# Optimization experiments

Measured on AMD Instinct MI355X. Metric: run time of the kernel, lower is better.

## Reference

```python
import jax, jax.numpy as jnp
import numpy as np

C, PH, PW, H, W = 10, 7, 7, 34, 34
STRIDE = 8.0
S = 4  # sample_per_part


def setup_inputs() -> dict:
    key = jax.random.key(0)
    k1, k2, k3, k4, k5 = jax.random.split(key, 5)
    N = 30000
    ft = jax.random.normal(k1, (1, C * PH * PW, H, W), dtype=jnp.float32)
    x1 = jax.random.uniform(k2, (N,), dtype=jnp.float32) * 200.0
    y1 = jax.random.uniform(k3, (N,), dtype=jnp.float32) * 200.0
    bw = jax.random.uniform(k4, (N,), dtype=jnp.float32) * 70.0 + 2.0
    bh = jax.random.uniform(k5, (N,), dtype=jnp.float32) * 70.0 + 2.0
    rois = jnp.stack([jnp.zeros((N,), jnp.float32), x1, y1, x1 + bw, y1 + bh], axis=1)
    return {"ft_add_left_right": ft, "rois": rois}


def reference(ft_add_left_right, rois):
    ft = ft_add_left_right[0].reshape(C, PH, PW, H, W)
    roi_start_w = rois[:, 1] / STRIDE
    roi_start_h = rois[:, 2] / STRIDE
    roi_end_w = rois[:, 3] / STRIDE
    roi_end_h = rois[:, 4] / STRIDE
    # torch.threshold(x, 0.1, 0.1): x if x > 0.1 else 0.1
    roi_height = jnp.where(roi_end_h - roi_start_h > 0.1, roi_end_h - roi_start_h, 0.1)
    roi_width = jnp.where(roi_end_w - roi_start_w > 0.1, roi_end_w - roi_start_w, 0.1)
    bin_size_h = roi_height / PH
    bin_size_w = roi_width / PW
    sub_h = bin_size_h / S
    sub_w = bin_size_w / S

    gh, gw = jnp.meshgrid(jnp.arange(PH), jnp.arange(PW), indexing='ij')
    phs = gh.reshape(-1, 1)  # [49,1]
    pws = gw.reshape(-1, 1)  # [49,1]
    hstart = jnp.floor(roi_start_h + phs * bin_size_h)  # [49,N]
    wstart = jnp.floor(roi_start_w + pws * bin_size_w)  # [49,N]

    N = rois.shape[0]
    sum_ = jnp.zeros((C, PH * PW, N), jnp.float32)
    count = jnp.zeros((PH * PW, N), jnp.float32)

    for ih in range(S):
        for iw in range(S):
            w = wstart + (iw + 0.5) * sub_w  # [49,N]
            h = hstart + (ih + 0.5) * sub_h
            keep = (w > -1) & (w < W) & (h > -1) & (h < H)
            x1 = jnp.floor(w).astype(jnp.int32)
            x2 = jnp.ceil(w).astype(jnp.int32)
            y1 = jnp.floor(h).astype(jnp.int32)
            y2 = jnp.ceil(h).astype(jnp.int32)
            x1v = (x1 >= 0) & (x1 < W)
            x2v = (x2 >= 0) & (x2 < W)
            y1v = (y1 >= 0) & (y1 < H)
            y2v = (y2 >= 0) & (y2 < H)
            x1 = jnp.clip(x1, 0, W - 1)
            x2 = jnp.clip(x2, 0, W - 1)
            y1 = jnp.clip(y1, 0, H - 1)
            y2 = jnp.clip(y2, 0, H - 1)
            dist_x = w - x1
            dist_y = h - y1
            # gathers: result [C,49,N]
            v11 = ft[:, phs, pws, y1, x1]
            v12 = ft[:, phs, pws, y2, x1]
            v21 = ft[:, phs, pws, y1, x2]
            v22 = ft[:, phs, pws, y2, x2]
            # faithful to source: ALL four masks zero value11 only (source bug)
            bad11 = (~x1v & y1v) | (~x1v & y2v) | (~x2v & y1v) | (~x2v & y2v)
            v11 = jnp.where(bad11, 0.0, v11)
            value = ((1 - dist_x) * (1 - dist_y) * v11
                     + (1 - dist_x) * dist_y * v12
                     + dist_x * (1 - dist_y) * v21
                     + dist_x * dist_y * v22)
            sum_ = sum_ + jnp.where(keep, value, 0.0)
            count = count + keep.astype(jnp.float32)

    out = jnp.where(count > 0, sum_ / jnp.maximum(count, 1.0), sum_)
    return jnp.transpose(out, (2, 0, 1))  # [N, C, 49]
```

## Files before the change

### kernel.cpp

```cpp
#include <hip/hip_runtime.h>


#define NC 10
#define NBIN 49
#define FH 34
#define FW 34
#define PLANE (FH * FW)
#define CSTRIDE 16
#define RPB 16
#define TSTRIDE 491

__global__ __launch_bounds__(256) void prep_kernel(
    const float* __restrict__ ft, float* __restrict__ ftT)
{
    const int p = blockIdx.x * 256 + threadIdx.x;
    if (p >= NBIN * PLANE) return;
    float v[NC];
#pragma unroll
    for (int c = 0; c < NC; ++c) v[c] = ft[c * (NBIN * PLANE) + p];
    float4* d = reinterpret_cast<float4*>(ftT + (size_t)p * CSTRIDE);
    d[0] = make_float4(v[0], v[1], v[2], v[3]);
    d[1] = make_float4(v[4], v[5], v[6], v[7]);
    d[2] = make_float4(v[8], v[9], 0.f, 0.f);
}

__global__ __launch_bounds__(256) void main_kernel(
    const float* __restrict__ rois, const float* __restrict__ ftT,
    const float* __restrict__ ft, float* __restrict__ out, int N, int use_t)
{
    __shared__ float tile[RPB][TSTRIDE];

    const int r = threadIdx.x & (RPB - 1);
    const int s = threadIdx.x >> 4;
    const int n = blockIdx.x * RPB + r;
    const bool valid = (n < N);

    float rsw = 0.f, rsh = 0.f, rew = 0.f, reh = 0.f;
    if (valid) {
        rsw = rois[n * 5 + 1] * 0.125f;
        rsh = rois[n * 5 + 2] * 0.125f;
        rew = rois[n * 5 + 3] * 0.125f;
        reh = rois[n * 5 + 4] * 0.125f;
    }
    float rheight = __fsub_rn(reh, rsh);
    if (!(rheight > 0.1f)) rheight = 0.1f;
    float rwidth = __fsub_rn(rew, rsw);
    if (!(rwidth > 0.1f)) rwidth = 0.1f;
    const float bsh   = __fdiv_rn(rheight, 7.0f);
    const float bsw   = __fdiv_rn(rwidth, 7.0f);
    const float sub_h = __fdiv_rn(bsh, 4.0f);
    const float sub_w = __fdiv_rn(bsw, 4.0f);

#pragma unroll
    for (int j = 0; j < 4; ++j) {
        const int bin = j * 16 + s;
        if (valid && bin < NBIN) {
            const int ph = bin / 7;
            const int pw = bin - ph * 7;
            const float hstart = floorf(__fadd_rn(rsh, __fmul_rn((float)ph, bsh)));
            const float wstart = floorf(__fadd_rn(rsw, __fmul_rn((float)pw, bsw)));

            float AY[3] = {0.f, 0.f, 0.f}, BY[3] = {0.f, 0.f, 0.f};
            float cntY = 0.f;
            int Y0 = 0;
#pragma unroll
            for (int ih = 0; ih < 4; ++ih) {
                const float h = __fadd_rn(hstart, __fmul_rn((float)ih + 0.5f, sub_h));
                const bool hok = (h > -1.0f) && (h < (float)FH);
                const int y1 = (int)floorf(h);
                const int y2 = (int)ceilf(h);
                const bool y1v = (y1 >= 0) && (y1 < FH);
                const bool y2v = (y2 >= 0) && (y2 < FH);
                const int y1c = min(max(y1, 0), FH - 1);
                const int y2c = min(max(y2, 0), FH - 1);
                const float dy = __fsub_rn(h, (float)y1c);
                if (ih == 0) Y0 = y1c;
                const int i1 = y1c - Y0, i2 = y2c - Y0;
                const float t1 = hok ? (1.0f - dy) : 0.0f;
                const float t2 = hok ? dy : 0.0f;
                const float tb = (hok && (y1v || y2v)) ? (1.0f - dy) : 0.0f;
                cntY += hok ? 1.0f : 0.0f;
#pragma unroll
                for (int p = 0; p < 3; ++p) {
                    AY[p] += (i1 == p) ? t1 : 0.0f;
                    AY[p] += (i2 == p) ? t2 : 0.0f;
                    BY[p] += (i1 == p) ? tb : 0.0f;
                }
            }

            float AX[3] = {0.f, 0.f, 0.f}, BX[3] = {0.f, 0.f, 0.f};
            float cntX = 0.f;
            int X0 = 0;
#pragma unroll
            for (int iw = 0; iw < 4; ++iw) {
                const float w = __fadd_rn(wstart, __fmul_rn((float)iw + 0.5f, sub_w));
                const bool wok = (w > -1.0f) && (w < (float)FW);
                const int x1 = (int)floorf(w);
                const int x2 = (int)ceilf(w);
                const bool x1v = (x1 >= 0) && (x1 < FW);
                const bool x2v = (x2 >= 0) && (x2 < FW);
                const int x1c = min(max(x1, 0), FW - 1);
                const int x2c = min(max(x2, 0), FW - 1);
                const float dx = __fsub_rn(w, (float)x1c);
                if (iw == 0) X0 = x1c;
                const int i1 = x1c - X0, i2 = x2c - X0;
                const float t1 = wok ? (1.0f - dx) : 0.0f;
                const float t2 = wok ? dx : 0.0f;
                const float tb = (wok && ((!x1v) || (!x2v))) ? (1.0f - dx) : 0.0f;
                cntX += wok ? 1.0f : 0.0f;
#pragma unroll
                for (int q = 0; q < 3; ++q) {
                    AX[q] += (i1 == q) ? t1 : 0.0f;
                    AX[q] += (i2 == q) ? t2 : 0.0f;
                    BX[q] += (i1 == q) ? tb : 0.0f;
                }
            }

            float sum[NC];
#pragma unroll
            for (int c = 0; c < NC; ++c) sum[c] = 0.f;

            const int binbase = bin * PLANE;
#pragma unroll
            for (int p = 0; p < 3; ++p) {
                const int py = min(Y0 + p, FH - 1);
#pragma unroll
                for (int q = 0; q < 3; ++q) {
                    const int px = min(X0 + q, FW - 1);
                    const float wgt = AY[p] * AX[q] - BY[p] * BX[q];
                    if (wgt != 0.0f) {
                        if (use_t) {
                            const float* pix = ftT + (size_t)(binbase + py * FW + px) * CSTRIDE;
                            const float4 a  = *(const float4*)pix;
                            const float4 b  = *(const float4*)(pix + 4);
                            const float2 c2 = *(const float2*)(pix + 8);
                            sum[0] += wgt * a.x;  sum[1] += wgt * a.y;
                            sum[2] += wgt * a.z;  sum[3] += wgt * a.w;
                            sum[4] += wgt * b.x;  sum[5] += wgt * b.y;
                            sum[6] += wgt * b.z;  sum[7] += wgt * b.w;
                            sum[8] += wgt * c2.x; sum[9] += wgt * c2.y;
                        } else {
                            const int off = binbase + py * FW + px;
#pragma unroll
                            for (int c = 0; c < NC; ++c)
                                sum[c] += wgt * ft[c * (NBIN * PLANE) + off];
                        }
                    }
                }
            }

            const float cnt = cntY * cntX;
            const float inv = (cnt > 0.0f) ? __fdiv_rn(1.0f, cnt) : 1.0f;
            float* tp = &tile[r][0];
#pragma unroll
            for (int c = 0; c < NC; ++c) tp[c * NBIN + bin] = sum[c] * inv;
        }
    }

    __syncthreads();

    const int n0 = blockIdx.x * RPB;
    for (int i = threadIdx.x; i < RPB * (NC * NBIN); i += 256) {
        const int row = i / (NC * NBIN);
        const int col = i - row * (NC * NBIN);
        const int n2 = n0 + row;
        if (n2 < N) out[(size_t)n2 * (NC * NBIN) + col] = tile[row][col];
    }
}

extern "C" void kernel_launch(void* const* d_in, const int* in_sizes, int n_in,
                              void* d_out, int out_size, void* d_ws, size_t ws_size,
                              hipStream_t stream) {
    const float* ft   = (const float*)d_in[0];
    const float* rois = (const float*)d_in[1];
    float* out        = (float*)d_out;
    const int N = in_sizes[1] / 5;

    const size_t need = (size_t)NBIN * PLANE * CSTRIDE * sizeof(float);
    const int use_t = (ws_size >= need) ? 1 : 0;
    float* ftT = (float*)d_ws;

    if (use_t) {
        const int npix = NBIN * PLANE;
        prep_kernel<<<(npix + 255) / 256, 256, 0, stream>>>(ft, ftT);
    }
    main_kernel<<<(N + RPB - 1) / RPB, 256, 0, stream>>>(rois, ftT, ft, out, N, use_t);
}
```

Measured before the change: 129.0 us.

## Share per-row/column interpolation weights via LDS and issue branchless gathers

```diff
diff --git a/kernel.cpp b/kernel.cpp
--- a/kernel.cpp
+++ b/kernel.cpp
@@ -9,6 +9,7 @@
 #define CSTRIDE 16
 #define RPB 16
 #define TSTRIDE 491
+#define NSIDE 14
 
 __global__ __launch_bounds__(256) void prep_kernel(
     const float* __restrict__ ft, float* __restrict__ ftT)
@@ -28,6 +29,7 @@
     const float* __restrict__ rois, const float* __restrict__ ftT,
     const float* __restrict__ ft, float* __restrict__ out, int N, int use_t)
 {
+    __shared__ float sides[NSIDE][RPB][8];
     __shared__ float tile[RPB][TSTRIDE];
 
     const int r = threadIdx.x & (RPB - 1);
@@ -51,101 +53,116 @@
     const float sub_h = __fdiv_rn(bsh, 4.0f);
     const float sub_w = __fdiv_rn(bsw, 4.0f);
 
+    if (s < NSIDE) {
+        const bool isY = (s < 7);
+        const int  k   = isY ? s : s - 7;
+        const float st = isY ? rsh : rsw;
+        const float bs = isY ? bsh : bsw;
+        const float sb = isY ? sub_h : sub_w;
+        const float start = floorf(__fadd_rn(st, __fmul_rn((float)k, bs)));
+
+        float A[3] = {0.f, 0.f, 0.f}, B[3] = {0.f, 0.f, 0.f};
+        float cnt = 0.f;
+        int P0 = 0;
+#pragma unroll
+        for (int i = 0; i < 4; ++i) {
+            const float h = __fadd_rn(start, __fmul_rn((float)i + 0.5f, sb));
+            const bool ok = (h > -1.0f) && (h < 34.0f);
+            const int p1 = (int)floorf(h);
+            const int p2 = (int)ceilf(h);
+            const bool v1 = (p1 >= 0) && (p1 < 34);
+            const bool v2 = (p2 >= 0) && (p2 < 34);
+            const int p1c = min(max(p1, 0), 33);
+            const int p2c = min(max(p2, 0), 33);
+            const float d = __fsub_rn(h, (float)p1c);
+            if (i == 0) P0 = p1c;
+            const int i1 = p1c - P0, i2 = p2c - P0;
+            const float t1 = ok ? (1.0f - d) : 0.0f;
+            const float t2 = ok ? d : 0.0f;
+            const bool bsel = isY ? (v1 || v2) : ((!v1) || (!v2));
+            const float tb = (ok && bsel) ? (1.0f - d) : 0.0f;
+            cnt += ok ? 1.0f : 0.0f;
+#pragma unroll
+            for (int p = 0; p < 3; ++p) {
+                A[p] += (i1 == p) ? t1 : 0.0f;
+                A[p] += (i2 == p) ? t2 : 0.0f;
+                B[p] += (i1 == p) ? tb : 0.0f;
+            }
+        }
+        float* sp = &sides[s][r][0];
+        sp[0] = A[0]; sp[1] = A[1]; sp[2] = A[2];
+        sp[3] = B[0]; sp[4] = B[1]; sp[5] = B[2];
+        sp[6] = cnt;  sp[7] = (float)P0;
+    }
+    __syncthreads();
+
 #pragma unroll
     for (int j = 0; j < 4; ++j) {
-        const int bin = j * 16 + s;
+        const int bin = j * RPB + s;
         if (valid && bin < NBIN) {
             const int ph = bin / 7;
             const int pw = bin - ph * 7;
-            const float hstart = floorf(__fadd_rn(rsh, __fmul_rn((float)ph, bsh)));
-            const float wstart = floorf(__fadd_rn(rsw, __fmul_rn((float)pw, bsw)));
-
-            float AY[3] = {0.f, 0.f, 0.f}, BY[3] = {0.f, 0.f, 0.f};
-            float cntY = 0.f;
-            int Y0 = 0;
-#pragma unroll
-            for (int ih = 0; ih < 4; ++ih) {
-                const float h = __fadd_rn(hstart, __fmul_rn((float)ih + 0.5f, sub_h));
-                const bool hok = (h > -1.0f) && (h < (float)FH);
-                const int y1 = (int)floorf(h);
-                const int y2 = (int)ceilf(h);
-                const bool y1v = (y1 >= 0) && (y1 < FH);
-                const bool y2v = (y2 >= 0) && (y2 < FH);
-                const int y1c = min(max(y1, 0), FH - 1);
-                const int y2c = min(max(y2, 0), FH - 1);
-                const float dy = __fsub_rn(h, (float)y1c);
-                if (ih == 0) Y0 = y1c;
-                const int i1 = y1c - Y0, i2 = y2c - Y0;
-                const float t1 = hok ? (1.0f - dy) : 0.0f;
-                const float t2 = hok ? dy : 0.0f;
-                const float tb = (hok && (y1v || y2v)) ? (1.0f - dy) : 0.0f;
-                cntY += hok ? 1.0f : 0.0f;
-#pragma unroll
-                for (int p = 0; p < 3; ++p) {
-                    AY[p] += (i1 == p) ? t1 : 0.0f;
-                    AY[p] += (i2 == p) ? t2 : 0.0f;
-                    BY[p] += (i1 == p) ? tb : 0.0f;
+
+            const float4 ya = *(const float4*)&sides[ph][r][0];
+            const float4 yb = *(const float4*)&sides[ph][r][4];
+            const float4 xa = *(const float4*)&sides[7 + pw][r][0];
+            const float4 xb = *(const float4*)&sides[7 + pw][r][4];
+            const float AY[3] = {ya.x, ya.y, ya.z};
+            const float BY[3] = {ya.w, yb.x, yb.y};
+            const float cntY  = yb.z;
+            const int   Y0    = (int)yb.w;
+            const float AX[3] = {xa.x, xa.y, xa.z};
+            const float BX[3] = {xa.w, xb.x, xb.y};
+            const float cntX  = xb.z;
+            const int   X0    = (int)xb.w;
+
+            const int binbase = bin * PLANE;
+            const int rowo[3] = {binbase + Y0 * FW,
+                                 binbase + min(Y0 + 1, FH - 1) * FW,
+                                 binbase + min(Y0 + 2, FH - 1) * FW};
+            const int colo[3] = {X0, min(X0 + 1, FW - 1), min(X0 + 2, FW - 1)};
+
+            float wgt[9];
+            int   off[9];
+#pragma unroll
+            for (int p = 0; p < 3; ++p)
+#pragma unroll
+                for (int q = 0; q < 3; ++q) {
+                    const float w = AY[p] * AX[q] - BY[p] * BX[q];
+                    wgt[3 * p + q] = w;
+                    off[3 * p + q] = (w != 0.0f) ? (rowo[p] + colo[q]) : binbase;
                 }
-            }
-
-            float AX[3] = {0.f, 0.f, 0.f}, BX[3] = {0.f, 0.f, 0.f};
-            float cntX = 0.f;
-            int X0 = 0;
-#pragma unroll
-            for (int iw = 0; iw < 4; ++iw) {
-                const float w = __fadd_rn(wstart, __fmul_rn((float)iw + 0.5f, sub_w));
-                const bool wok = (w > -1.0f) && (w < (float)FW);
-                const int x1 = (int)floorf(w);
-                const int x2 = (int)ceilf(w);
-                const bool x1v = (x1 >= 0) && (x1 < FW);
-                const bool x2v = (x2 >= 0) && (x2 < FW);
-                const int x1c = min(max(x1, 0), FW - 1);
-                const int x2c = min(max(x2, 0), FW - 1);
-                const float dx = __fsub_rn(w, (float)x1c);
-                if (iw == 0) X0 = x1c;
-                const int i1 = x1c - X0, i2 = x2c - X0;
-                const float t1 = wok ? (1.0f - dx) : 0.0f;
-                const float t2 = wok ? dx : 0.0f;
-                const float tb = (wok && ((!x1v) || (!x2v))) ? (1.0f - dx) : 0.0f;
-                cntX += wok ? 1.0f : 0.0f;
-#pragma unroll
-                for (int q = 0; q < 3; ++q) {
-                    AX[q] += (i1 == q) ? t1 : 0.0f;
-                    AX[q] += (i2 == q) ? t2 : 0.0f;
-                    BX[q] += (i1 == q) ? tb : 0.0f;
+
+            float sum[NC];
+#pragma unroll
+            for (int c = 0; c < NC; ++c) sum[c] = 0.f;
+
+            if (use_t) {
+#pragma unroll
+                for (int k = 0; k < 9; ++k) {
+                    const float* pix = ftT + (size_t)off[k] * CSTRIDE;
+                    const float4 a  = *(const float4*)pix;
+                    const float4 b  = *(const float4*)(pix + 4);
+                    const float2 c2 = *(const float2*)(pix + 8);
+                    const float w = wgt[k];
+                    sum[0] = fmaf(w, a.x, sum[0]);
+                    sum[1] = fmaf(w, a.y, sum[1]);
+                    sum[2] = fmaf(w, a.z, sum[2]);
+                    sum[3] = fmaf(w, a.w, sum[3]);
+                    sum[4] = fmaf(w, b.x, sum[4]);
+                    sum[5] = fmaf(w, b.y, sum[5]);
+                    sum[6] = fmaf(w, b.z, sum[6]);
+                    sum[7] = fmaf(w, b.w, sum[7]);
+                    sum[8] = fmaf(w, c2.x, sum[8]);
+                    sum[9] = fmaf(w, c2.y, sum[9]);
                 }
-            }
-
-            float sum[NC];
-#pragma unroll
-            for (int c = 0; c < NC; ++c) sum[c] = 0.f;
-
-            const int binbase = bin * PLANE;
-#pragma unroll
-            for (int p = 0; p < 3; ++p) {
-                const int py = min(Y0 + p, FH - 1);
-#pragma unroll
-                for (int q = 0; q < 3; ++q) {
-                    const int px = min(X0 + q, FW - 1);
-                    const float wgt = AY[p] * AX[q] - BY[p] * BX[q];
-                    if (wgt != 0.0f) {
-                        if (use_t) {
-                            const float* pix = ftT + (size_t)(binbase + py * FW + px) * CSTRIDE;
-                            const float4 a  = *(const float4*)pix;
-                            const float4 b  = *(const float4*)(pix + 4);
-                            const float2 c2 = *(const float2*)(pix + 8);
-                            sum[0] += wgt * a.x;  sum[1] += wgt * a.y;
-                            sum[2] += wgt * a.z;  sum[3] += wgt * a.w;
-                            sum[4] += wgt * b.x;  sum[5] += wgt * b.y;
-                            sum[6] += wgt * b.z;  sum[7] += wgt * b.w;
-                            sum[8] += wgt * c2.x; sum[9] += wgt * c2.y;
-                        } else {
-                            const int off = binbase + py * FW + px;
-#pragma unroll
-                            for (int c = 0; c < NC; ++c)
-                                sum[c] += wgt * ft[c * (NBIN * PLANE) + off];
-                        }
-                    }
+            } else {
+#pragma unroll
+                for (int k = 0; k < 9; ++k) {
+                    const float w = wgt[k];
+#pragma unroll
+                    for (int c = 0; c < NC; ++c)
+                        sum[c] = fmaf(w, ft[c * (NBIN * PLANE) + off[k]], sum[c]);
                 }
             }
 
```

After: 125.8 us. 2.5% less time.
